# Optimization experiments

Measured on AMD Instinct MI355X. Metric: run time of the kernel, lower is better.

Reference implementation:

```python
import jax, jax.numpy as jnp
import numpy as np

EPS = 1e-5
B, S, D = 4, 2048, 128
BALL_SCALE = 0.05  # keeps points inside the unit Poincare ball for c=1


def setup_inputs() -> dict:
    key = jax.random.key(0)
    kq, kk, kv = jax.random.split(key, 3)
    q = jax.random.normal(kq, (B, S, D), dtype=jnp.float32) * BALL_SCALE
    k = jax.random.normal(kk, (B, S, D), dtype=jnp.float32) * BALL_SCALE
    v_tangent = jax.random.normal(kv, (B, S, D), dtype=jnp.float32)
    c = jnp.asarray(1.0, dtype=jnp.float32)
    beta = jnp.asarray(0.0, dtype=jnp.float32)            # nn.Parameter init 0.0
    attention_bias = jnp.asarray(0.0, dtype=jnp.float32)  # nn.Parameter init 0.0
    return {"q": q, "k": k, "v_tangent": v_tangent, "c": c,
            "beta": beta, "attention_bias": attention_bias}


def reference(q, k, v_tangent, c, beta, attention_bias):
    sqrt_c = jnp.sqrt(c)

    # --- pairwise Poincare distance (all fp32, as in the torch autocast block) ---
    x_norm_sq = jnp.sum(q * q, axis=-1, keepdims=True)            # (B,S,1)
    y_norm_sq = jnp.sum(k * k, axis=-1, keepdims=True)            # (B,S,1)
    xy_dot = jnp.einsum('bsd,btd->bst', q, k)                     # (B,S,S)
    y_norm_sq_t = jnp.swapaxes(y_norm_sq, -2, -1)                 # (B,1,S)
    diff_norm_sq = x_norm_sq - 2.0 * xy_dot + y_norm_sq_t         # ||x-y||^2, (B,S,S)
    denom = (1.0 - c * x_norm_sq) * (1.0 - c * y_norm_sq_t)       # (B,S,S)
    arg = 1.0 + 2.0 * c * diff_norm_sq / jnp.maximum(denom, EPS)
    dist = jnp.arccosh(jnp.maximum(arg, 1.0 + EPS)) / sqrt_c      # (B,S,S)

    # --- attention ---
    beta_positive = jax.nn.softplus(beta)
    attention_scores = -beta_positive * dist - attention_bias
    attention_weights = jax.nn.softmax(attention_scores, axis=-1)  # (B,S,S)
    output_tangent = jnp.einsum('bst,btd->bsd', attention_weights, v_tangent)

    # --- exp map at origin ---
    v_norm = jnp.maximum(
        jnp.sqrt(jnp.sum(output_tangent * output_tangent, axis=-1, keepdims=True)), EPS)
    output_hyperbolic = (jnp.tanh(sqrt_c * v_norm) / sqrt_c) * (output_tangent / v_norm)

    return output_hyperbolic, attention_weights
```

## Files before the change

### kernel.cpp

```cpp
#include <hip/hip_runtime.h>
#include <math.h>

#define B_ 4
#define S_ 2048
#define D_ 128
#define EPSF 1e-5f
#define BN 128
#define PSB 272

typedef __attribute__((ext_vector_type(8))) short short8;
typedef __attribute__((ext_vector_type(4))) float f32x4;

static __device__ __forceinline__ unsigned short f2bf(float f) {
    unsigned u = __float_as_uint(f);
    return (unsigned short)((u + 0x7fffu + ((u >> 16) & 1u)) >> 16);
}

static __device__ __forceinline__ void gload_lds16(const void* g, void* l) {
    __builtin_amdgcn_global_load_lds((const __attribute__((address_space(1))) unsigned*)g,
                                     (__attribute__((address_space(3))) unsigned*)l, 16, 0, 0);
}


__global__ __launch_bounds__(256) void convqk_kernel(const float* __restrict__ q,
                                                     const float* __restrict__ k,
                                                     float* __restrict__ qn, float* __restrict__ kn,
                                                     float* __restrict__ lws,
                                                     unsigned* __restrict__ Qb, unsigned* __restrict__ Kb) {
    int row = blockIdx.x * 4 + (threadIdx.x >> 6);
    int lane = threadIdx.x & 63;
    const int NR = B_ * S_;
    bool isQ = row < NR;
    int r = isQ ? row : row - NR;
    float2 v = ((const float2*)(isQ ? q : k))[(size_t)r * 64 + lane];
    unsigned pk = (unsigned)f2bf(v.x) | ((unsigned)f2bf(v.y) << 16);
    float nrm = v.x * v.x + v.y * v.y;
#pragma unroll
    for (int m = 1; m <= 32; m <<= 1) nrm += __shfl_xor(nrm, m, 64);
    if (isQ) {
        Qb[(size_t)r * 64 + lane] = pk;
        if (lane == 0) qn[r] = nrm;
        if (lane == 1) lws[r] = 0.f;
    } else {
        int c = lane >> 2;
        int cs = c ^ (r & 7);
        Kb[(size_t)r * 64 + cs * 4 + (lane & 3)] = pk;
        if (lane == 0) kn[r] = nrm;
    }
}

__global__ __launch_bounds__(256) void convv_kernel(const float* __restrict__ v, uint4* __restrict__ Vtb) {
    __shared__ unsigned short Vs[128 * 132];
    int b = blockIdx.x >> 4;
    int t = blockIdx.x & 15;
    int tid = threadIdx.x;
    const float* src = v + ((size_t)b * S_ + t * 128) * D_;
    int d4 = tid & 31, key0 = tid >> 5;
#pragma unroll
    for (int it = 0; it < 16; ++it) {
        int key = key0 + it * 8;
        float4 f = *(const float4*)(src + (size_t)key * D_ + d4 * 4);
        unsigned short* dst = &Vs[key * 132 + d4 * 4];
        dst[0] = f2bf(f.x); dst[1] = f2bf(f.y); dst[2] = f2bf(f.z); dst[3] = f2bf(f.w);
    }
    __syncthreads();
    uint4* tile = Vtb + (size_t)blockIdx.x * (128 * 16);
    int d = tid & 127;
    int cl = tid >> 7;
#pragma unroll
    for (int it = 0; it < 8; ++it) {
        int c = cl + it * 2;
        int kb = c * 8;
        unsigned short e0 = Vs[(kb + 0) * 132 + d], e1 = Vs[(kb + 1) * 132 + d];
        unsigned short e2 = Vs[(kb + 2) * 132 + d], e3 = Vs[(kb + 3) * 132 + d];
        unsigned short e4 = Vs[(kb + 4) * 132 + d], e5 = Vs[(kb + 5) * 132 + d];
        unsigned short e6 = Vs[(kb + 6) * 132 + d], e7 = Vs[(kb + 7) * 132 + d];
        uint4 o;
        o.x = (unsigned)e0 | ((unsigned)e1 << 16);
        o.y = (unsigned)e2 | ((unsigned)e3 << 16);
        o.z = (unsigned)e4 | ((unsigned)e5 << 16);
        o.w = (unsigned)e6 | ((unsigned)e7 << 16);
        tile[d * 16 + (c ^ (d & 7))] = o;
    }
}


__global__ __launch_bounds__(512, 2) void hattn2_kernel(
    const unsigned short* __restrict__ Qb, const char* __restrict__ Kb, const char* __restrict__ Vtb,
    const float* __restrict__ qn, const float* __restrict__ kn,
    const float* __restrict__ cp, const float* __restrict__ betap, const float* __restrict__ biasp,
    float* __restrict__ lws, float* __restrict__ Opart, uint4* __restrict__ Pws) {

    __shared__ __align__(1024) char smem[76032];
    char* KsB = smem;
    char* VtB = smem + 32768;
    char* PsB = smem + 65536;
    float* yn_s  = (float*)(smem + 74240);
    float* gy_s  = (float*)(smem + 74752);
    float* xn_s  = (float*)(smem + 75264);
    float* rx_s  = (float*)(smem + 75392);
    float* l_row = (float*)(smem + 75520);

    const int tid = threadIdx.x;
    const int lane = tid & 63, wave = tid >> 6;
    const int wm = wave & 1, wn = wave >> 1;
    const int lm = lane & 15, quad = lane >> 4;

    const int th = blockIdx.x & 1;
    const int b = (blockIdx.x >> 1) & 3;
    const int rb = blockIdx.x >> 3;
    const int s0 = rb * 32;
    const size_t bS = (size_t)b * S_;

    const float cc = cp[0], beta = betap[0], bias = biasp[0];
    const float beta_pos = fmaxf(beta, 0.f) + log1pf(__expf(-fabsf(beta)));
    const float sqrt_c = sqrtf(cc);
    const float bneg = -beta_pos / sqrt_c;
    const float bias2 = -bias * 1.442695040888963f;
    const float onepe = 1.f + EPSF;
    const float c2 = 2.f * cc;

    if (tid < 32) {
        float xn = qn[bS + s0 + tid];
        xn_s[tid] = xn;
        rx_s[tid] = c2 * __builtin_amdgcn_rcpf(1.f - cc * xn);
        l_row[tid] = 0.f;
    }

    short8 aq[4];
    {
        const unsigned short* qrow = Qb + (bS + s0 + wm * 16 + lm) * D_;
#pragma unroll
        for (int ks = 0; ks < 4; ++ks)
            aq[ks] = *(const short8*)(qrow + ks * 32 + quad * 8);
    }

    f32x4 o0 = {0.f, 0.f, 0.f, 0.f}, o1 = {0.f, 0.f, 0.f, 0.f};

    const char* KbBase = Kb + bS * 256;
    const char* VtBase = Vtb + (size_t)b * 16 * 32768;

    for (int it = 0; it < 8; ++it) {
        int t = th * 8 + it;
        int t0 = t * BN;
        __syncthreads();
        {
            const char* ks = KbBase + (size_t)t0 * 256;
            const char* vs = VtBase + (size_t)t * 32768;
#pragma unroll
            for (int j = 0; j < 4; ++j) {
                int off = (tid + j * 512) * 16;
                gload_lds16(ks + off, KsB + off);
                gload_lds16(vs + off, VtB + off);
            }
            if (tid < BN) {
                float yn = kn[bS + t0 + tid];
                yn_s[tid] = yn;
                gy_s[tid] = __builtin_amdgcn_rcpf(1.f - cc * yn);
            }
        }
        __syncthreads();

        f32x4 acc0 = {0.f, 0.f, 0.f, 0.f}, acc1 = {0.f, 0.f, 0.f, 0.f};
#pragma unroll
        for (int ks = 0; ks < 4; ++ks) {
            int n0 = wn * 32 + lm;
            int c = ks * 4 + quad;
            short8 b0 = *(const short8*)(KsB + n0 * 256 + ((c ^ (n0 & 7)) * 16));
            int n1 = n0 + 16;
            short8 b1 = *(const short8*)(KsB + n1 * 256 + ((c ^ (n1 & 7)) * 16));
            acc0 = __builtin_amdgcn_mfma_f32_16x16x32_bf16(aq[ks], b0, acc0, 0, 0, 0);
            acc1 = __builtin_amdgcn_mfma_f32_16x16x32_bf16(aq[ks], b1, acc1, 0, 0, 0);
        }

        int col0 = wn * 32 + lm, col1 = col0 + 16;
        float yn0 = yn_s[col0], gy0 = gy_s[col0];
        float yn1 = yn_s[col1], gy1 = gy_s[col1];
#pragma unroll
        for (int r = 0; r < 4; ++r) {
            int row = wm * 16 + quad * 4 + r;
            float xn = xn_s[row];
            float rx = rx_s[row];

            float diff0 = fmaf(-2.f, acc0[r], xn + yn0);
            float arg0 = fmaf(diff0 * gy0, rx, 1.f);
            arg0 = fmaxf(arg0, onepe);
            float w0 = arg0 + sqrtf(fmaf(arg0, arg0, -1.f));
            float p0 = __builtin_amdgcn_exp2f(fmaf(bneg, __builtin_amdgcn_logf(w0), bias2));

            float diff1 = fmaf(-2.f, acc1[r], xn + yn1);
            float arg1 = fmaf(diff1 * gy1, rx, 1.f);
            arg1 = fmaxf(arg1, onepe);
            float w1 = arg1 + sqrtf(fmaf(arg1, arg1, -1.f));
            float p1 = __builtin_amdgcn_exp2f(fmaf(bneg, __builtin_amdgcn_logf(w1), bias2));

            *(unsigned short*)(PsB + row * PSB + col0 * 2) = f2bf(p0);
            *(unsigned short*)(PsB + row * PSB + col1 * 2) = f2bf(p1);

            float s = p0 + p1;
#pragma unroll
            for (int m = 1; m <= 8; m <<= 1) s += __shfl_xor(s, m, 64);
            if (lm == 0) atomicAdd(&l_row[row], s);
        }
        __syncthreads();

        {
            int row = tid >> 4, chunk = tid & 15;
            uint4 pv = *(const uint4*)(PsB + row * PSB + chunk * 16);
            Pws[(((bS + s0 + row) * S_ + t0) >> 3) + chunk] = pv;
        }

#pragma unroll
        for (int ks = 0; ks < 4; ++ks) {
            short8 ap = *(const short8*)(PsB + (wm * 16 + lm) * PSB + (ks * 32 + quad * 8) * 2);
            int d0 = wn * 32 + lm;
            int c = ks * 4 + quad;
            short8 v0 = *(const short8*)(VtB + d0 * 256 + ((c ^ (d0 & 7)) * 16));
            int d1 = d0 + 16;
            short8 v1 = *(const short8*)(VtB + d1 * 256 + ((c ^ (d1 & 7)) * 16));
            o0 = __builtin_amdgcn_mfma_f32_16x16x32_bf16(ap, v0, o0, 0, 0, 0);
            o1 = __builtin_amdgcn_mfma_f32_16x16x32_bf16(ap, v1, o1, 0, 0, 0);
        }
    }
    __syncthreads();

    float* op = Opart + (size_t)th * (B_ * S_ * D_) + (bS + s0) * D_;
#pragma unroll
    for (int r = 0; r < 4; ++r) {
        int row = wm * 16 + quad * 4 + r;
        op[(size_t)row * D_ + wn * 32 + lm] = o0[r];
        op[(size_t)row * D_ + wn * 32 + 16 + lm] = o1[r];
    }
    if (tid < 32) atomicAdd(&lws[bS + s0 + tid], l_row[tid]);
}

__global__ __launch_bounds__(256) void hepi_kernel(const float* __restrict__ Opart,
                                                   const float* __restrict__ lws,
                                                   const float* __restrict__ cp,
                                                   float* __restrict__ hout) {
    int row = blockIdx.x * 4 + (threadIdx.x >> 6);
    int lane = threadIdx.x & 63;
    const float cc = cp[0];
    const float sqrt_c = sqrtf(cc);
    float2 a = ((const float2*)(Opart + (size_t)row * D_))[lane];
    float2 b = ((const float2*)(Opart + (size_t)(B_ * S_ * D_) + (size_t)row * D_))[lane];
    float linv = 1.f / lws[row];
    float x0 = (a.x + b.x) * linv;
    float x1 = (a.y + b.y) * linv;
    float np = x0 * x0 + x1 * x1;
#pragma unroll
    for (int m = 1; m <= 32; m <<= 1) np += __shfl_xor(np, m, 64);
    float vn = fmaxf(sqrtf(np), EPSF);
    float aa = sqrt_c * vn;
    float t = 1.f - 2.f / (__expf(2.f * aa) + 1.f);
    float sc = t / aa;
    float2 o = {x0 * sc, x1 * sc};
    ((float2*)(hout + (size_t)row * D_))[lane] = o;
}

__global__ __launch_bounds__(256) void wnorm2_kernel(const uint4* __restrict__ Pws,
                                                     const float* __restrict__ lws,
                                                     float* __restrict__ w) {
    size_t idx = (size_t)blockIdx.x * 256 + threadIdx.x;
    int row = (int)(idx >> 8);
    float linv = 1.f / lws[row];
    uint4 u = Pws[idx];
    float4 f0, f1;
    f0.x = __uint_as_float(u.x << 16) * linv;
    f0.y = __uint_as_float(u.x & 0xffff0000u) * linv;
    f0.z = __uint_as_float(u.y << 16) * linv;
    f0.w = __uint_as_float(u.y & 0xffff0000u) * linv;
    f1.x = __uint_as_float(u.z << 16) * linv;
    f1.y = __uint_as_float(u.z & 0xffff0000u) * linv;
    f1.z = __uint_as_float(u.w << 16) * linv;
    f1.w = __uint_as_float(u.w & 0xffff0000u) * linv;
    float4* out = (float4*)w + idx * 2;
    out[0] = f0;
    out[1] = f1;
}


__global__ __launch_bounds__(512, 2) void hattn_kernel(
    const unsigned short* __restrict__ Qb, const char* __restrict__ Kb, const char* __restrict__ Vtb,
    const float* __restrict__ qn, const float* __restrict__ kn,
    const float* __restrict__ cp, const float* __restrict__ betap, const float* __restrict__ biasp,
    float* __restrict__ lws, float* __restrict__ houtg, float* __restrict__ woutg) {

    __shared__ __align__(1024) char smem[75136];
    char* KsB = smem;
    char* VtB = smem + 32768;
    char* PsB = smem + 65536;
    float* kn_s  = (float*)(smem + 74240);
    float* qn_s  = (float*)(smem + 74752);
    float* l_row = (float*)(smem + 74880);
    float* nsq_s = (float*)(smem + 75008);

    const int tid = threadIdx.x;
    const int lane = tid & 63, wave = tid >> 6;
    const int wm = wave & 1, wn = wave >> 1;
    const int lm = lane & 15, quad = lane >> 4;

    int xcd = blockIdx.x & 7;
    int b = xcd >> 1;
    int rb = (blockIdx.x >> 3) * 2 + (xcd & 1);
    int s0 = rb * 32;
    const size_t bS = (size_t)b * S_;

    const float cc = cp[0], beta = betap[0], bias = biasp[0];
    const float beta_pos = fmaxf(beta, 0.f) + log1pf(__expf(-fabsf(beta)));
    const float sqrt_c = sqrtf(cc);
    const float inv_sqrt_c = 1.f / sqrt_c;

    if (tid < 32) {
        qn_s[tid] = qn[bS + s0 + tid];
        l_row[tid] = 0.f;
        nsq_s[tid] = 0.f;
    }

    short8 aq[4];
    {
        const unsigned short* qrow = Qb + (bS + s0 + wm * 16 + lm) * D_;
#pragma unroll
        for (int ks = 0; ks < 4; ++ks)
            aq[ks] = *(const short8*)(qrow + ks * 32 + quad * 8);
    }

    f32x4 o0 = {0.f, 0.f, 0.f, 0.f}, o1 = {0.f, 0.f, 0.f, 0.f};

    const char* KbBase = Kb + bS * 256;
    const char* VtBase = Vtb + (size_t)b * 16 * 32768;

    for (int t = 0; t < S_ / BN; ++t) {
        int t0 = t * BN;
        __syncthreads();
        {
            const uint4* ksrc = (const uint4*)(KbBase + (size_t)t0 * 256);
            const uint4* vsrc = (const uint4*)(VtBase + (size_t)t * 32768);
            uint4* kd = (uint4*)KsB;
            uint4* vd = (uint4*)VtB;
#pragma unroll
            for (int i = 0; i < 4; ++i) {
                kd[tid + i * 512] = ksrc[tid + i * 512];
                vd[tid + i * 512] = vsrc[tid + i * 512];
            }
            if (tid < BN) kn_s[tid] = kn[bS + t0 + tid];
        }
        __syncthreads();

        f32x4 acc0 = {0.f, 0.f, 0.f, 0.f}, acc1 = {0.f, 0.f, 0.f, 0.f};
#pragma unroll
        for (int ks = 0; ks < 4; ++ks) {
            int n0 = wn * 32 + lm;
            int c = ks * 4 + quad;
            short8 b0 = *(const short8*)(KsB + n0 * 256 + ((c ^ (n0 & 7)) * 16));
            int n1 = n0 + 16;
            short8 b1 = *(const short8*)(KsB + n1 * 256 + ((c ^ (n1 & 7)) * 16));
            acc0 = __builtin_amdgcn_mfma_f32_16x16x32_bf16(aq[ks], b0, acc0, 0, 0, 0);
            acc1 = __builtin_amdgcn_mfma_f32_16x16x32_bf16(aq[ks], b1, acc1, 0, 0, 0);
        }

        float lp[4];
#pragma unroll
        for (int r = 0; r < 4; ++r) {
            int row = wm * 16 + quad * 4 + r;
            float xn = qn_s[row];
            float fx = 1.f - cc * xn;
            float p0, p1;
#pragma unroll
            for (int nt = 0; nt < 2; ++nt) {
                int col = wn * 32 + nt * 16 + lm;
                float dot = (nt == 0) ? acc0[r] : acc1[r];
                float yn = kn_s[col];
                float diff = xn - 2.f * dot + yn;
                float den = fmaxf(fx * (1.f - cc * yn), EPSF);
                float arg = fmaf(2.f * cc * diff, __builtin_amdgcn_rcpf(den), 1.f);
                arg = fmaxf(arg, 1.f + EPSF);
                float dist = __logf(arg + sqrtf(arg * arg - 1.f)) * inv_sqrt_c;
                float p = __expf(fmaf(-beta_pos, dist, -bias));
                woutg[(bS + s0 + row) * S_ + t0 + col] = p;
                *(unsigned short*)(PsB + row * PSB + col * 2) = f2bf(p);
                if (nt == 0) p0 = p; else p1 = p;
            }
            lp[r] = p0 + p1;
        }
#pragma unroll
        for (int r = 0; r < 4; ++r) {
            float s = lp[r];
#pragma unroll
            for (int m = 1; m <= 8; m <<= 1) s += __shfl_xor(s, m, 64);
            if (lm == 0) atomicAdd(&l_row[wm * 16 + quad * 4 + r], s);
        }
        __syncthreads();

#pragma unroll
        for (int ks = 0; ks < 4; ++ks) {
            short8 ap = *(const short8*)(PsB + (wm * 16 + lm) * PSB + (ks * 32 + quad * 8) * 2);
            int d0 = wn * 32 + lm;
            int c = ks * 4 + quad;
            short8 v0 = *(const short8*)(VtB + d0 * 256 + ((c ^ (d0 & 7)) * 16));
            int d1 = d0 + 16;
            short8 v1 = *(const short8*)(VtB + d1 * 256 + ((c ^ (d1 & 7)) * 16));
            o0 = __builtin_amdgcn_mfma_f32_16x16x32_bf16(ap, v0, o0, 0, 0, 0);
            o1 = __builtin_amdgcn_mfma_f32_16x16x32_bf16(ap, v1, o1, 0, 0, 0);
        }
    }
    __syncthreads();

    float xs0[4], xs1[4];
#pragma unroll
    for (int r = 0; r < 4; ++r) {
        int row = wm * 16 + quad * 4 + r;
        float linv = __builtin_amdgcn_rcpf(l_row[row]);
        float x0 = o0[r] * linv, x1 = o1[r] * linv;
        xs0[r] = x0; xs1[r] = x1;
        float np = x0 * x0 + x1 * x1;
#pragma unroll
        for (int m = 1; m <= 8; m <<= 1) np += __shfl_xor(np, m, 64);
        if (lm == 0) atomicAdd(&nsq_s[row], np);
    }
    if (tid < 32) lws[bS + s0 + tid] = l_row[tid];
    __syncthreads();
#pragma unroll
    for (int r = 0; r < 4; ++r) {
        int row = wm * 16 + quad * 4 + r;
        float vn = fmaxf(sqrtf(nsq_s[row]), EPSF);
        float a = sqrt_c * vn;
        float th = 1.f - 2.f * __builtin_amdgcn_rcpf(__expf(2.f * a) + 1.f);
        float sc = th / a;
        houtg[(bS + s0 + row) * D_ + wn * 32 + lm] = xs0[r] * sc;
        houtg[(bS + s0 + row) * D_ + wn * 32 + 16 + lm] = xs1[r] * sc;
    }
}

__global__ __launch_bounds__(256) void wnorm_kernel(float* __restrict__ w,
                                                    const float* __restrict__ lws) {
    size_t idx = (size_t)blockIdx.x * 256 + threadIdx.x;
    int row = (int)(idx >> 9);
    float linv = 1.f / lws[row];
    float4* p = (float4*)w + idx;
    float4 v = *p;
    v.x *= linv; v.y *= linv; v.z *= linv; v.w *= linv;
    *p = v;
}


extern "C" void kernel_launch(void* const* d_in, const int* in_sizes, int n_in,
                              void* d_out, int out_size, void* d_ws, size_t ws_size,
                              hipStream_t stream) {
    const float* q    = (const float*)d_in[0];
    const float* k    = (const float*)d_in[1];
    const float* v    = (const float*)d_in[2];
    const float* c    = (const float*)d_in[3];
    const float* beta = (const float*)d_in[4];
    const float* ab   = (const float*)d_in[5];

    float* out  = (float*)d_out;
    float* hout = out;
    float* wout = out + (size_t)B_ * S_ * D_;

    float* qn  = (float*)d_ws;
    float* kn  = qn + B_ * S_;
    float* lws = kn + B_ * S_;
    char*  wsb = (char*)d_ws;
    const size_t QB_OFF = 98304;
    const size_t KB_OFF = QB_OFF + 2097152;
    const size_t VT_OFF = KB_OFF + 2097152;
    const size_t NEED1  = VT_OFF + 2097152;
    const size_t OP_OFF = NEED1;
    const size_t PW_OFF = OP_OFF + 2u * B_ * S_ * D_ * 4;
    const size_t NEED2  = PW_OFF + (size_t)B_ * S_ * S_ * 2;

    unsigned* Qb = (unsigned*)(wsb + QB_OFF);
    unsigned* Kb = (unsigned*)(wsb + KB_OFF);
    uint4*   Vtb = (uint4*)(wsb + VT_OFF);

    if (ws_size >= NEED2) {
        float* Opart = (float*)(wsb + OP_OFF);
        uint4* Pws   = (uint4*)(wsb + PW_OFF);
        convqk_kernel<<<4096, 256, 0, stream>>>(q, k, qn, kn, lws, Qb, Kb);
        convv_kernel<<<64, 256, 0, stream>>>(v, Vtb);
        hattn2_kernel<<<512, 512, 0, stream>>>((const unsigned short*)Qb, (const char*)Kb,
                                               (const char*)Vtb, qn, kn, c, beta, ab,
                                               lws, Opart, Pws);
        hepi_kernel<<<2048, 256, 0, stream>>>(Opart, lws, c, hout);
        wnorm2_kernel<<<8192, 256, 0, stream>>>(Pws, lws, wout);
    } else {
        convqk_kernel<<<4096, 256, 0, stream>>>(q, k, qn, kn, lws, Qb, Kb);
        convv_kernel<<<64, 256, 0, stream>>>(v, Vtb);
        hattn_kernel<<<256, 512, 0, stream>>>((const unsigned short*)Qb, (const char*)Kb,
                                              (const char*)Vtb, qn, kn, c, beta, ab,
                                              lws, hout, wout);
        wnorm_kernel<<<(B_ * S_ * S_ / 4) / 256, 256, 0, stream>>>(wout, lws);
    }
}
```

Measured before the change: 148.6 us.

## Double-buffer K/V tiles with 64-key steps and precompute per-row norm factors

The attention kernel now processes 64-key tiles in a double-buffered LDS ring. The next K tile is prefetched before the QK MFMA and the next V tile after the softmax stage, so global loads overlap compute instead of sitting between barriers. The per-row norm and reciprocal factors move into the conversion kernel as packed float2, and row sums are accumulated in registers and reduced once at the end instead of with per-tile LDS atomics. In exchange there are twice as many iterations with their barriers, and each wave issues fewer MFMAs per tile.

```diff
diff --git a/kernel.cpp b/kernel.cpp
--- a/kernel.cpp
+++ b/kernel.cpp
@@ -6,6 +6,7 @@
 #define D_ 128
 #define EPSF 1e-5f
 #define BN 128
+#define BN2 64
 #define PSB 272
 
 typedef __attribute__((ext_vector_type(8))) short short8;
@@ -24,12 +25,15 @@
 
 __global__ __launch_bounds__(256) void convqk_kernel(const float* __restrict__ q,
                                                      const float* __restrict__ k,
+                                                     const float* __restrict__ cp,
                                                      float* __restrict__ qn, float* __restrict__ kn,
                                                      float* __restrict__ lws,
+                                                     float2* __restrict__ qng, float2* __restrict__ kng,
                                                      unsigned* __restrict__ Qb, unsigned* __restrict__ Kb) {
     int row = blockIdx.x * 4 + (threadIdx.x >> 6);
     int lane = threadIdx.x & 63;
     const int NR = B_ * S_;
+    const float cc = cp[0];
     bool isQ = row < NR;
     int r = isQ ? row : row - NR;
     float2 v = ((const float2*)(isQ ? q : k))[(size_t)r * 64 + lane];
@@ -39,13 +43,19 @@
     for (int m = 1; m <= 32; m <<= 1) nrm += __shfl_xor(nrm, m, 64);
     if (isQ) {
         Qb[(size_t)r * 64 + lane] = pk;
-        if (lane == 0) qn[r] = nrm;
+        if (lane == 0) {
+            qn[r] = nrm;
+            qng[r] = make_float2(nrm, 2.f * cc * __builtin_amdgcn_rcpf(1.f - cc * nrm));
+        }
         if (lane == 1) lws[r] = 0.f;
     } else {
         int c = lane >> 2;
         int cs = c ^ (r & 7);
         Kb[(size_t)r * 64 + cs * 4 + (lane & 3)] = pk;
-        if (lane == 0) kn[r] = nrm;
+        if (lane == 0) {
+            kn[r] = nrm;
+            kng[r] = make_float2(nrm, __builtin_amdgcn_rcpf(1.f - cc * nrm));
+        }
     }
 }
 
@@ -85,20 +95,14 @@
 }
 
 
-__global__ __launch_bounds__(512, 2) void hattn2_kernel(
+__global__ __launch_bounds__(512, 2) void hattn3_kernel(
     const unsigned short* __restrict__ Qb, const char* __restrict__ Kb, const char* __restrict__ Vtb,
-    const float* __restrict__ qn, const float* __restrict__ kn,
+    const float2* __restrict__ qng, const float2* __restrict__ kng,
     const float* __restrict__ cp, const float* __restrict__ betap, const float* __restrict__ biasp,
     float* __restrict__ lws, float* __restrict__ Opart, uint4* __restrict__ Pws) {
 
-    __shared__ __align__(1024) char smem[76032];
-    char* KsB = smem;
-    char* VtB = smem + 32768;
+    __shared__ __align__(1024) char smem[75648];
     char* PsB = smem + 65536;
-    float* yn_s  = (float*)(smem + 74240);
-    float* gy_s  = (float*)(smem + 74752);
-    float* xn_s  = (float*)(smem + 75264);
-    float* rx_s  = (float*)(smem + 75392);
     float* l_row = (float*)(smem + 75520);
 
     const int tid = threadIdx.x;
@@ -111,20 +115,37 @@
     const int rb = blockIdx.x >> 3;
     const int s0 = rb * 32;
     const size_t bS = (size_t)b * S_;
-
-    const float cc = cp[0], beta = betap[0], bias = biasp[0];
+    const int g0 = th * 16;
+
+    const float beta = betap[0], bias = biasp[0];
+    const float cc = cp[0];
     const float beta_pos = fmaxf(beta, 0.f) + log1pf(__expf(-fabsf(beta)));
     const float sqrt_c = sqrtf(cc);
     const float bneg = -beta_pos / sqrt_c;
     const float bias2 = -bias * 1.442695040888963f;
     const float onepe = 1.f + EPSF;
-    const float c2 = 2.f * cc;
-
-    if (tid < 32) {
-        float xn = qn[bS + s0 + tid];
-        xn_s[tid] = xn;
-        rx_s[tid] = c2 * __builtin_amdgcn_rcpf(1.f - cc * xn);
-        l_row[tid] = 0.f;
+
+    const char* KbBase = Kb + bS * 256;
+    const char* VtBase = Vtb + (size_t)b * 16 * 32768;
+
+    {
+        const char* ks = KbBase + (size_t)g0 * 16384;
+        const char* vs = VtBase + (size_t)(g0 >> 1) * 32768 + (size_t)(g0 & 1) * 128;
+#pragma unroll
+        for (int j = 0; j < 2; ++j) {
+            int m = tid + j * 512;
+            gload_lds16(ks + m * 16, smem + m * 16);
+            gload_lds16(vs + (m >> 3) * 256 + (m & 7) * 16, smem + 32768 + m * 16);
+        }
+        if (tid < 64) {
+            float2 y = kng[bS + (size_t)g0 * 64 + tid];
+            *(float2*)(smem + 74240 + tid * 8) = y;
+        }
+        if (tid >= 64 && tid < 96) {
+            float2 x = qng[bS + s0 + (tid - 64)];
+            *(float2*)(smem + 75264 + (tid - 64) * 8) = x;
+        }
+        if (tid >= 96 && tid < 128) l_row[tid - 96] = 0.f;
     }
 
     short8 aq[4];
@@ -136,91 +157,94 @@
     }
 
     f32x4 o0 = {0.f, 0.f, 0.f, 0.f}, o1 = {0.f, 0.f, 0.f, 0.f};
-
-    const char* KbBase = Kb + bS * 256;
-    const char* VtBase = Vtb + (size_t)b * 16 * 32768;
-
-    for (int it = 0; it < 8; ++it) {
-        int t = th * 8 + it;
-        int t0 = t * BN;
+    float lacc[4] = {0.f, 0.f, 0.f, 0.f};
+
+    __syncthreads();
+
+    int p = 0;
+    const int n0 = wn * 16 + lm;
+    for (int it = 0; it < 16; ++it) {
+        char* KsC = smem + p * 16384;
+        char* VtC = smem + 32768 + p * 16384;
+        const char* YGC = smem + 74240 + p * 512;
+
+        float2 ygn;
+        if (it < 15) {
+            int g = g0 + it + 1;
+            const char* ks = KbBase + (size_t)g * 16384;
+            char* kd = smem + (p ^ 1) * 16384;
+#pragma unroll
+            for (int j = 0; j < 2; ++j) {
+                int off = (tid + j * 512) * 16;
+                gload_lds16(ks + off, kd + off);
+            }
+            if (tid < 64) ygn = kng[bS + (size_t)g * 64 + tid];
+        }
+
+        f32x4 acc = {0.f, 0.f, 0.f, 0.f};
+#pragma unroll
+        for (int ks = 0; ks < 4; ++ks) {
+            int c = ks * 4 + quad;
+            short8 bk = *(const short8*)(KsC + n0 * 256 + ((c ^ (n0 & 7)) * 16));
+            acc = __builtin_amdgcn_mfma_f32_16x16x32_bf16(aq[ks], bk, acc, 0, 0, 0);
+        }
+
+        {
+            float2 yg = *(const float2*)(YGC + n0 * 8);
+#pragma unroll
+            for (int r = 0; r < 4; ++r) {
+                int row = wm * 16 + quad * 4 + r;
+                float2 xr = *(const float2*)(smem + 75264 + row * 8);
+                float diff = fmaf(-2.f, acc[r], xr.x + yg.x);
+                float arg = fmaf(diff * yg.y, xr.y, 1.f);
+                arg = fmaxf(arg, onepe);
+                float w = arg + sqrtf(fmaf(arg, arg, -1.f));
+                float pv = __builtin_amdgcn_exp2f(fmaf(bneg, __builtin_amdgcn_logf(w), bias2));
+                *(unsigned short*)(PsB + row * PSB + n0 * 2) = f2bf(pv);
+                lacc[r] += pv;
+            }
+        }
         __syncthreads();
-        {
-            const char* ks = KbBase + (size_t)t0 * 256;
-            const char* vs = VtBase + (size_t)t * 32768;
-#pragma unroll
-            for (int j = 0; j < 4; ++j) {
-                int off = (tid + j * 512) * 16;
-                gload_lds16(ks + off, KsB + off);
-                gload_lds16(vs + off, VtB + off);
+
+        if (it < 15) {
+            int g = g0 + it + 1;
+            const char* vs = VtBase + (size_t)(g >> 1) * 32768 + (size_t)(g & 1) * 128;
+            char* vd = smem + 32768 + (p ^ 1) * 16384;
+#pragma unroll
+            for (int j = 0; j < 2; ++j) {
+                int m = tid + j * 512;
+                gload_lds16(vs + (m >> 3) * 256 + (m & 7) * 16, vd + m * 16);
             }
-            if (tid < BN) {
-                float yn = kn[bS + t0 + tid];
-                yn_s[tid] = yn;
-                gy_s[tid] = __builtin_amdgcn_rcpf(1.f - cc * yn);
-            }
-        }
-        __syncthreads();
-
-        f32x4 acc0 = {0.f, 0.f, 0.f, 0.f}, acc1 = {0.f, 0.f, 0.f, 0.f};
-#pragma unroll
-        for (int ks = 0; ks < 4; ++ks) {
-            int n0 = wn * 32 + lm;
-            int c = ks * 4 + quad;
-            short8 b0 = *(const short8*)(KsB + n0 * 256 + ((c ^ (n0 & 7)) * 16));
-            int n1 = n0 + 16;
-            short8 b1 = *(const short8*)(KsB + n1 * 256 + ((c ^ (n1 & 7)) * 16));
-            acc0 = __builtin_amdgcn_mfma_f32_16x16x32_bf16(aq[ks], b0, acc0, 0, 0, 0);
-            acc1 = __builtin_amdgcn_mfma_f32_16x16x32_bf16(aq[ks], b1, acc1, 0, 0, 0);
-        }
-
-        int col0 = wn * 32 + lm, col1 = col0 + 16;
-        float yn0 = yn_s[col0], gy0 = gy_s[col0];
-        float yn1 = yn_s[col1], gy1 = gy_s[col1];
-#pragma unroll
-        for (int r = 0; r < 4; ++r) {
-            int row = wm * 16 + quad * 4 + r;
-            float xn = xn_s[row];
-            float rx = rx_s[row];
-
-            float diff0 = fmaf(-2.f, acc0[r], xn + yn0);
-            float arg0 = fmaf(diff0 * gy0, rx, 1.f);
-            arg0 = fmaxf(arg0, onepe);
-            float w0 = arg0 + sqrtf(fmaf(arg0, arg0, -1.f));
-            float p0 = __builtin_amdgcn_exp2f(fmaf(bneg, __builtin_amdgcn_logf(w0), bias2));
-
-            float diff1 = fmaf(-2.f, acc1[r], xn + yn1);
-            float arg1 = fmaf(diff1 * gy1, rx, 1.f);
-            arg1 = fmaxf(arg1, onepe);
-            float w1 = arg1 + sqrtf(fmaf(arg1, arg1, -1.f));
-            float p1 = __builtin_amdgcn_exp2f(fmaf(bneg, __builtin_amdgcn_logf(w1), bias2));
-
-            *(unsigned short*)(PsB + row * PSB + col0 * 2) = f2bf(p0);
-            *(unsigned short*)(PsB + row * PSB + col1 * 2) = f2bf(p1);
-
-            float s = p0 + p1;
-#pragma unroll
-            for (int m = 1; m <= 8; m <<= 1) s += __shfl_xor(s, m, 64);
-            if (lm == 0) atomicAdd(&l_row[row], s);
-        }
-        __syncthreads();
-
-        {
-            int row = tid >> 4, chunk = tid & 15;
-            uint4 pv = *(const uint4*)(PsB + row * PSB + chunk * 16);
-            Pws[(((bS + s0 + row) * S_ + t0) >> 3) + chunk] = pv;
-        }
-
-#pragma unroll
-        for (int ks = 0; ks < 4; ++ks) {
-            short8 ap = *(const short8*)(PsB + (wm * 16 + lm) * PSB + (ks * 32 + quad * 8) * 2);
+            if (tid < 64) *(float2*)(smem + 74240 + (p ^ 1) * 512 + tid * 8) = ygn;
+        }
+
+        if (tid < 256) {
+            int row = tid >> 3, ch = tid & 7;
+            uint4 pv = *(const uint4*)(PsB + row * PSB + ch * 16);
+            Pws[(((bS + s0 + row) * S_ + (size_t)(g0 + it) * 64) >> 3) + ch] = pv;
+        }
+
+#pragma unroll
+        for (int ks2 = 0; ks2 < 2; ++ks2) {
+            short8 ap = *(const short8*)(PsB + (wm * 16 + lm) * PSB + (ks2 * 32 + quad * 8) * 2);
             int d0 = wn * 32 + lm;
-            int c = ks * 4 + quad;
-            short8 v0 = *(const short8*)(VtB + d0 * 256 + ((c ^ (d0 & 7)) * 16));
+            int lo = ks2 * 4 + quad;
+            short8 v0 = *(const short8*)(VtC + d0 * 128 + ((lo ^ (d0 & 7)) * 16));
             int d1 = d0 + 16;
-            short8 v1 = *(const short8*)(VtB + d1 * 256 + ((c ^ (d1 & 7)) * 16));
+            short8 v1 = *(const short8*)(VtC + d1 * 128 + ((lo ^ (d1 & 7)) * 16));
             o0 = __builtin_amdgcn_mfma_f32_16x16x32_bf16(ap, v0, o0, 0, 0, 0);
             o1 = __builtin_amdgcn_mfma_f32_16x16x32_bf16(ap, v1, o1, 0, 0, 0);
         }
+        __syncthreads();
+        p ^= 1;
+    }
+
+#pragma unroll
+    for (int r = 0; r < 4; ++r) {
+        float s = lacc[r];
+#pragma unroll
+        for (int m = 1; m <= 8; m <<= 1) s += __shfl_xor(s, m, 64);
+        if (lm == 0) atomicAdd(&l_row[wm * 16 + quad * 4 + r], s);
     }
     __syncthreads();
 
@@ -462,7 +486,9 @@
     float* kn  = qn + B_ * S_;
     float* lws = kn + B_ * S_;
     char*  wsb = (char*)d_ws;
-    const size_t QB_OFF = 98304;
+    const size_t QG_OFF = 98304;
+    const size_t KG_OFF = QG_OFF + 65536;
+    const size_t QB_OFF = KG_OFF + 65536;
     const size_t KB_OFF = QB_OFF + 2097152;
     const size_t VT_OFF = KB_OFF + 2097152;
     const size_t NEED1  = VT_OFF + 2097152;
@@ -470,6 +496,8 @@
     const size_t PW_OFF = OP_OFF + 2u * B_ * S_ * D_ * 4;
     const size_t NEED2  = PW_OFF + (size_t)B_ * S_ * S_ * 2;
 
+    float2*  qng = (float2*)(wsb + QG_OFF);
+    float2*  kng = (float2*)(wsb + KG_OFF);
     unsigned* Qb = (unsigned*)(wsb + QB_OFF);
     unsigned* Kb = (unsigned*)(wsb + KB_OFF);
     uint4*   Vtb = (uint4*)(wsb + VT_OFF);
@@ -477,15 +505,15 @@
     if (ws_size >= NEED2) {
         float* Opart = (float*)(wsb + OP_OFF);
         uint4* Pws   = (uint4*)(wsb + PW_OFF);
-        convqk_kernel<<<4096, 256, 0, stream>>>(q, k, qn, kn, lws, Qb, Kb);
+        convqk_kernel<<<4096, 256, 0, stream>>>(q, k, c, qn, kn, lws, qng, kng, Qb, Kb);
         convv_kernel<<<64, 256, 0, stream>>>(v, Vtb);
-        hattn2_kernel<<<512, 512, 0, stream>>>((const unsigned short*)Qb, (const char*)Kb,
-                                               (const char*)Vtb, qn, kn, c, beta, ab,
+        hattn3_kernel<<<512, 512, 0, stream>>>((const unsigned short*)Qb, (const char*)Kb,
+                                               (const char*)Vtb, qng, kng, c, beta, ab,
                                                lws, Opart, Pws);
         hepi_kernel<<<2048, 256, 0, stream>>>(Opart, lws, c, hout);
         wnorm2_kernel<<<8192, 256, 0, stream>>>(Pws, lws, wout);
     } else {
-        convqk_kernel<<<4096, 256, 0, stream>>>(q, k, qn, kn, lws, Qb, Kb);
+        convqk_kernel<<<4096, 256, 0, stream>>>(q, k, c, qn, kn, lws, qng, kng, Qb, Kb);
         convv_kernel<<<64, 256, 0, stream>>>(v, Vtb);
         hattn_kernel<<<256, 512, 0, stream>>>((const unsigned short*)Qb, (const char*)Kb,
                                               (const char*)Vtb, qn, kn, c, beta, ab,
```

New measurement: 141.5 us. -4.8%, faster.
